# Performance work log

Measured on AMD Instinct MI355X. Metric: run time of the kernel, lower is better.

Reference implementation:

```python
import jax, jax.numpy as jnp
import numpy as np

NEG_INF = np.float32(-np.inf)

def setup_inputs() -> dict:
    key = jax.random.key(0)
    k1, k2 = jax.random.split(key)
    x = jax.random.normal(k1, (8, 4, 512, 512), dtype=jnp.float32)
    weight = jax.random.normal(k2, (8, 4, 5, 5), dtype=jnp.float32)
    return {"x": x, "weight": weight}

def reference(x, weight):
    # Morphological (max-plus) dilation:
    # out[n,co,h,w] = max_{ci,kh,kw} x[n,ci,h+kh-oh, w+kw-ow] + weight[co,ci,kh,kw]
    # origin (oh,ow) = kernel_size // 2; out-of-bounds -> padding_value (-inf).
    N, Ci, H, W = x.shape
    Co, _, Kh, Kw = weight.shape
    oh, ow = Kh // 2, Kw // 2
    xp = jnp.pad(x, ((0, 0), (0, 0), (oh, Kh - 1 - oh), (ow, Kw - 1 - ow)),
                 constant_values=NEG_INF)
    out = jnp.full((N, Co, H, W), NEG_INF, dtype=x.dtype)
    # small fixed loop over the Kh*Kw structuring-element taps; data dims vectorized
    for kh in range(Kh):
        for kw in range(Kw):
            win = xp[:, :, kh:kh + H, kw:kw + W]            # [N,Ci,H,W]
            w_tap = weight[:, :, kh, kw]                     # [Co,Ci]
            cand = jnp.max(win[:, None] + w_tap[None, :, :, None, None], axis=2)  # [N,Co,H,W]
            out = jnp.maximum(out, cand)
    return out
```

## Files before the change

### kernel.cpp

```cpp
#include <hip/hip_runtime.h>

#define NEG_INF (-__builtin_inff())

__global__ __launch_bounds__(256, 4) void dil2d_kernel(const float* __restrict__ x,
                                                       const float* __restrict__ w,
                                                       float* __restrict__ out) {
    const int Ci = 4, H = 512, W = 512;

    const int tid = threadIdx.x;
    const int wg  = tid & 63;
    const int w0  = wg << 3;
    const int coh = (tid >> 6) & 1;
    const int rib = tid >> 7;
    const int co0 = __builtin_amdgcn_readfirstlane(coh << 2);
    const int b   = blockIdx.x;
    const int n   = b >> 8;
    const int h   = ((b & 255) << 1) + rib;

    float acc[4][8];
#pragma unroll
    for (int cs = 0; cs < 4; ++cs)
#pragma unroll
        for (int j = 0; j < 8; ++j) acc[cs][j] = NEG_INF;

    const float* xn = x + n * (Ci * H * W);

    const bool lo_edge = (w0 == 0);
    const bool hi_edge = (w0 == 504);
    const int  off_lo  = lo_edge ? 0   : (w0 - 4);
    const int  off_hi  = hi_edge ? 504 : (w0 + 8);

    for (int ci = 0; ci < Ci; ++ci) {
        const float* xc  = xn + ci * (H * W);
        const float* wci = w + co0 * (Ci * 25) + ci * 25;
        for (int kh = 0; kh < 5; ++kh) {
            const int r = h + kh - 2;
            if (r < 0 || r >= H) continue;
            const float* xr = xc + r * W;

            const float4 lo4 = *(const float4*)(xr + off_lo);
            const float4 m0  = *(const float4*)(xr + w0);
            const float4 m1  = *(const float4*)(xr + w0 + 4);
            const float4 hi4 = *(const float4*)(xr + off_hi);

            float xv[12];
            xv[0]  = lo_edge ? NEG_INF : lo4.z;
            xv[1]  = lo_edge ? NEG_INF : lo4.w;
            xv[2]  = m0.x; xv[3] = m0.y; xv[4] = m0.z; xv[5] = m0.w;
            xv[6]  = m1.x; xv[7] = m1.y; xv[8] = m1.z; xv[9] = m1.w;
            xv[10] = hi_edge ? NEG_INF : hi4.x;
            xv[11] = hi_edge ? NEG_INF : hi4.y;

            const float* wk = wci + kh * 5;
#pragma unroll
            for (int cs = 0; cs < 4; ++cs) {
                const float* wco = wk + cs * (Ci * 25);
                const float wv0 = wco[0], wv1 = wco[1], wv2 = wco[2],
                            wv3 = wco[3], wv4 = wco[4];
#pragma unroll
                for (int j = 0; j < 8; ++j) {
                    float m  = acc[cs][j];
                    float t0 = xv[j]     + wv0;
                    float t1 = xv[j + 1] + wv1;
                    m = fmaxf(m, fmaxf(t0, t1));
                    float t2 = xv[j + 2] + wv2;
                    float t3 = xv[j + 3] + wv3;
                    m = fmaxf(m, fmaxf(t2, t3));
                    m = fmaxf(m, xv[j + 4] + wv4);
                    acc[cs][j] = m;
                }
            }
        }
    }

    float* on = out + n * (8 * H * W) + (co0) * (H * W) + h * W + w0;
#pragma unroll
    for (int cs = 0; cs < 4; ++cs) {
        float* o = on + cs * (H * W);
        *(float4*)(o)     = make_float4(acc[cs][0], acc[cs][1], acc[cs][2], acc[cs][3]);
        *(float4*)(o + 4) = make_float4(acc[cs][4], acc[cs][5], acc[cs][6], acc[cs][7]);
    }
}

extern "C" void kernel_launch(void* const* d_in, const int* in_sizes, int n_in,
                              void* d_out, int out_size, void* d_ws, size_t ws_size,
                              hipStream_t stream) {
    const float* x = (const float*)d_in[0];
    const float* w = (const float*)d_in[1];
    float* out     = (float*)d_out;

    dim3 grid(2048), block(256);
    hipLaunchKernelGGL(dil2d_kernel, grid, block, 0, stream, x, w, out);
}
```

Baseline: 138.6 us.

## Split work across more blocks with 2 out-channels per wave and v_max3

Each wavefront now computes 2 output channels for one row instead of 4 output channels, and each block covers a single row with all 4 waves taking different channel pairs. The grid doubles to cover the same output. The inner max chain uses inline v_max3_f32 assembly, and the ci/kh loops are fully unrolled. This raises parallelism and cuts per-thread accumulator registers, at the cost of loading each input row for more waves, which increases redundant global and L2 traffic.

```diff
diff --git a/kernel.cpp b/kernel.cpp
--- a/kernel.cpp
+++ b/kernel.cpp
@@ -1,6 +1,12 @@
 #include <hip/hip_runtime.h>
 
 #define NEG_INF (-__builtin_inff())
+
+static __device__ __forceinline__ float max3f(float a, float b, float c) {
+    float d;
+    asm("v_max3_f32 %0, %1, %2, %3" : "=v"(d) : "v"(a), "v"(b), "v"(c));
+    return d;
+}
 
 __global__ __launch_bounds__(256, 4) void dil2d_kernel(const float* __restrict__ x,
                                                        const float* __restrict__ w,
@@ -10,16 +16,14 @@
     const int tid = threadIdx.x;
     const int wg  = tid & 63;
     const int w0  = wg << 3;
-    const int coh = (tid >> 6) & 1;
-    const int rib = tid >> 7;
-    const int co0 = __builtin_amdgcn_readfirstlane(coh << 2);
+    const int co0 = __builtin_amdgcn_readfirstlane((tid >> 6) << 1);
     const int b   = blockIdx.x;
-    const int n   = b >> 8;
-    const int h   = ((b & 255) << 1) + rib;
+    const int n   = b >> 9;
+    const int h   = b & 511;
 
-    float acc[4][8];
+    float acc[2][8];
 #pragma unroll
-    for (int cs = 0; cs < 4; ++cs)
+    for (int cs = 0; cs < 2; ++cs)
 #pragma unroll
         for (int j = 0; j < 8; ++j) acc[cs][j] = NEG_INF;
 
@@ -30,9 +34,11 @@
     const int  off_lo  = lo_edge ? 0   : (w0 - 4);
     const int  off_hi  = hi_edge ? 504 : (w0 + 8);
 
+#pragma unroll
     for (int ci = 0; ci < Ci; ++ci) {
         const float* xc  = xn + ci * (H * W);
-        const float* wci = w + co0 * (Ci * 25) + ci * 25;
+        const float* wci = w + (co0 * Ci + ci) * 25;
+#pragma unroll
         for (int kh = 0; kh < 5; ++kh) {
             const int r = h + kh - 2;
             if (r < 0 || r >= H) continue;
@@ -53,29 +59,30 @@
 
             const float* wk = wci + kh * 5;
 #pragma unroll
-            for (int cs = 0; cs < 4; ++cs) {
+            for (int cs = 0; cs < 2; ++cs) {
                 const float* wco = wk + cs * (Ci * 25);
                 const float wv0 = wco[0], wv1 = wco[1], wv2 = wco[2],
                             wv3 = wco[3], wv4 = wco[4];
 #pragma unroll
                 for (int j = 0; j < 8; ++j) {
-                    float m  = acc[cs][j];
-                    float t0 = xv[j]     + wv0;
-                    float t1 = xv[j + 1] + wv1;
-                    m = fmaxf(m, fmaxf(t0, t1));
-                    float t2 = xv[j + 2] + wv2;
-                    float t3 = xv[j + 3] + wv3;
-                    m = fmaxf(m, fmaxf(t2, t3));
-                    m = fmaxf(m, xv[j + 4] + wv4);
+                    const float t0 = xv[j]     + wv0;
+                    const float t1 = xv[j + 1] + wv1;
+                    const float t2 = xv[j + 2] + wv2;
+                    const float t3 = xv[j + 3] + wv3;
+                    const float t4 = xv[j + 4] + wv4;
+                    float m = acc[cs][j];
+                    m = max3f(m, t0, t1);
+                    m = max3f(m, t2, t3);
+                    m = fmaxf(m, t4);
                     acc[cs][j] = m;
                 }
             }
         }
     }
 
-    float* on = out + n * (8 * H * W) + (co0) * (H * W) + h * W + w0;
+    float* on = out + n * (8 * H * W) + co0 * (H * W) + h * W + w0;
 #pragma unroll
-    for (int cs = 0; cs < 4; ++cs) {
+    for (int cs = 0; cs < 2; ++cs) {
         float* o = on + cs * (H * W);
         *(float4*)(o)     = make_float4(acc[cs][0], acc[cs][1], acc[cs][2], acc[cs][3]);
         *(float4*)(o + 4) = make_float4(acc[cs][4], acc[cs][5], acc[cs][6], acc[cs][7]);
@@ -89,6 +96,6 @@
     const float* w = (const float*)d_in[1];
     float* out     = (float*)d_out;
 
-    dim3 grid(2048), block(256);
+    dim3 grid(4096), block(256);
     hipLaunchKernelGGL(dil2d_kernel, grid, block, 0, stream, x, w, out);
 }
```

Measured after the change: 143.0 us. +3.2%, slower.
